# Optimization experiments

Hardware: AMD Instinct MI355X
Metric: run time of the kernel (lower is better)

Reference implementation:

```python
import jax, jax.numpy as jnp
import numpy as np

NP, NC, F, H = 50000, 10000, 128, 256
E_ANNO, E_LINK, E_PPI, NPAIR = 250000, 100000, 500000, 4096


def _sage(x_src, x_dst, src, dst, Wl, b, Wr):
    # PyG SAGEConv(aggr='mean'): lin_l(mean of gathered neighbor feats) + lin_r(x_dst)
    n_dst = x_dst.shape[0]
    agg = jax.ops.segment_sum(x_src[src], dst, num_segments=n_dst)
    cnt = jax.ops.segment_sum(jnp.ones((src.shape[0], 1), x_src.dtype), dst, num_segments=n_dst)
    mean = agg / jnp.maximum(cnt, 1.0)  # isolated dst nodes get 0
    return mean @ Wl.T + b + x_dst @ Wr.T


def setup_inputs():
    key = jax.random.key(0)
    ks = iter(jax.random.split(key, 64))
    s = 0.05
    inp = {}
    inp['x_protein'] = jax.random.normal(next(ks), (NP, F), jnp.float32)
    inp['x_class'] = jax.random.normal(next(ks), (NC, F), jnp.float32)
    for layer, din, dout in [('a', F, H), ('b', H, F)]:
        for rel in ['annop', 'annon', 'link', 'ppi']:
            inp[f'{layer}_{rel}_Wl'] = jax.random.normal(next(ks), (dout, din), jnp.float32) * s
            inp[f'{layer}_{rel}_b'] = jax.random.normal(next(ks), (dout,), jnp.float32) * s
            inp[f'{layer}_{rel}_Wr'] = jax.random.normal(next(ks), (dout, din), jnp.float32) * s
    inp['lin_W'] = jax.random.normal(next(ks), (1, 2 * F), jnp.float32) * s
    inp['lin_b'] = jnp.zeros((1,), jnp.float32)
    inp['annop_src'] = jax.random.randint(next(ks), (E_ANNO,), 0, NP)
    inp['annop_dst'] = jax.random.randint(next(ks), (E_ANNO,), 0, NC)
    inp['annon_src'] = jax.random.randint(next(ks), (E_ANNO,), 0, NP)
    inp['annon_dst'] = jax.random.randint(next(ks), (E_ANNO,), 0, NC)
    inp['link_src'] = jax.random.randint(next(ks), (E_LINK,), 0, NC)
    inp['link_dst'] = jax.random.randint(next(ks), (E_LINK,), 0, NC)
    inp['ppi_src'] = jax.random.randint(next(ks), (E_PPI,), 0, NP)
    inp['ppi_dst'] = jax.random.randint(next(ks), (E_PPI,), 0, NP)
    inp['mask'] = jax.random.randint(next(ks), (NPAIR, 2), 0, NP)
    return inp


def reference(x_protein, x_class,
              a_annop_Wl, a_annop_b, a_annop_Wr,
              a_annon_Wl, a_annon_b, a_annon_Wr,
              a_link_Wl, a_link_b, a_link_Wr,
              a_ppi_Wl, a_ppi_b, a_ppi_Wr,
              b_annop_Wl, b_annop_b, b_annop_Wr,
              b_annon_Wl, b_annon_b, b_annon_Wr,
              b_link_Wl, b_link_b, b_link_Wr,
              b_ppi_Wl, b_ppi_b, b_ppi_Wr,
              lin_W, lin_b,
              annop_src, annop_dst, annon_src, annon_dst,
              link_src, link_dst, ppi_src, ppi_dst, mask):
    # Layer 1 (HeteroConv aggregates per dst node type with sum)
    hc = (_sage(x_protein, x_class, annop_src, annop_dst, a_annop_Wl, a_annop_b, a_annop_Wr)
          + _sage(x_protein, x_class, annon_src, annon_dst, a_annon_Wl, a_annon_b, a_annon_Wr)
          + _sage(x_class, x_class, link_src, link_dst, a_link_Wl, a_link_b, a_link_Wr))
    hp = _sage(x_protein, x_protein, ppi_src, ppi_dst, a_ppi_Wl, a_ppi_b, a_ppi_Wr)
    hc = jax.nn.relu(hc)
    hp = jax.nn.relu(hp)
    # Layer 2
    hp2 = _sage(hp, hp, ppi_src, ppi_dst, b_ppi_Wl, b_ppi_b, b_ppi_Wr)
    # (class outputs of layer 2 are computed in the original but unused for the head)
    hc2 = (_sage(hp, hc, annop_src, annop_dst, b_annop_Wl, b_annop_b, b_annop_Wr)
           + _sage(hp, hc, annon_src, annon_dst, b_annon_Wl, b_annon_b, b_annon_Wr)
           + _sage(hc, hc, link_src, link_dst, b_link_Wl, b_link_b, b_link_Wr))
    del hc2
    # Pair readout: mask.T -> rows of protein indices; original detaches p1, p2
    p1 = jax.lax.stop_gradient(hp2[mask[:, 0]])
    p2 = jax.lax.stop_gradient(hp2[mask[:, 1]])
    h = jnp.concatenate((p1, p2), axis=1)  # [NPAIR, 2F]
    return jax.nn.sigmoid(h @ lin_W.T + lin_b)
```

## Files before the change

kernel.cpp:

```cpp
#include <hip/hip_runtime.h>
#include <math.h>

#define NPROT 50000
#define NPROT_PAD 50048
#define EPPI 500000
#define NPAIR 4096

typedef __attribute__((ext_vector_type(8))) __bf16 bf16x8;
typedef __attribute__((ext_vector_type(4))) __bf16 bf16x4;
typedef __attribute__((ext_vector_type(4))) float floatx4;

__global__ void k_prep(const float* __restrict__ x,
                       const float* __restrict__ Wl, const float* __restrict__ Wr,
                       const float* __restrict__ linW, const float* __restrict__ linb,
                       const float* __restrict__ bWl, const float* __restrict__ bWr,
                       const float* __restrict__ bb,
                       __bf16* __restrict__ Xb, __bf16* __restrict__ Bw,
                       float* __restrict__ P, float* __restrict__ biasC,
                       int* __restrict__ head) {
    int b = blockIdx.x, t = threadIdx.x;
    if (b < 6250) {
        int i = b * 256 + t;
        int row = i >> 5, k4 = (i & 31) << 2;
        float4 v = *(const float4*)(x + (size_t)row * 128 + k4);
        bf16x4 o; o[0] = (__bf16)v.x; o[1] = (__bf16)v.y; o[2] = (__bf16)v.z; o[3] = (__bf16)v.w;
        *(bf16x4*)(Xb + (size_t)row * 128 + k4) = o;
    } else if (b < 6506) {
        int idx = (b - 6250) * 256 + t;
        int h = idx >> 8, k = idx & 255;
        float v = (k < 128) ? Wl[h * 128 + k] : Wr[h * 128 + (k - 128)];
        Bw[idx] = (__bf16)v;
    } else if (b == 6506) {
        int h = t;
        float v1 = 0, v2 = 0, u1 = 0, u2 = 0;
        for (int f = 0; f < 128; f++) {
            float w1 = linW[f], w2 = linW[128 + f];
            float wl = bWl[f * 256 + h], wr = bWr[f * 256 + h];
            v1 += w1 * wl; v2 += w2 * wl; u1 += w1 * wr; u2 += w2 * wr;
        }
        P[h * 4 + 0] = v1; P[h * 4 + 1] = v2; P[h * 4 + 2] = u1; P[h * 4 + 3] = u2;
        if (h == 0) {
            float c = linb[0];
            for (int f = 0; f < 128; f++) c += (linW[f] + linW[128 + f]) * bb[f];
            *biasC = c;
        }
    } else {
        int i = (b - 6507) * 256 + t;
        if (i < NPROT) head[i] = -1;
    }
}

__global__ void k_link(const int* __restrict__ src, const int* __restrict__ dst,
                       int* __restrict__ head, int2* __restrict__ elist) {
    int e = blockIdx.x * 256 + threadIdx.x;
    if (e < EPPI) {
        int d = dst[e];
        int prev = atomicExch(&head[d], e);
        elist[e] = make_int2(src[e], prev);
    }
}

__global__ void k_agg(const __bf16* __restrict__ Xb, const int* __restrict__ head,
                      const int2* __restrict__ elist, float* __restrict__ inv,
                      __bf16* __restrict__ Am) {
    int wave = threadIdx.x >> 6, lane = threadIdx.x & 63;
    int q = lane >> 4, sl = lane & 15;
    int node = blockIdx.x * 16 + wave * 4 + q;
    if (node >= NPROT) return;
    float a[8];
#pragma unroll
    for (int e8 = 0; e8 < 8; e8++) a[e8] = 0.f;
    const __bf16* base = Xb + (size_t)sl * 8;
    int e = head[node];
    int c = 0;
    while (e >= 0) {
        int2 el = elist[e];
        bf16x8 v = *(const bf16x8*)(base + (size_t)el.x * 128);
#pragma unroll
        for (int e8 = 0; e8 < 8; e8++) a[e8] += (float)v[e8];
        c++;
        e = el.y;
    }
    float iv = 1.0f / (float)(c > 1 ? c : 1);
    if (sl == 0 && q == 0) {  }
    if (sl == 0) inv[node] = iv;
    bf16x8 o;
#pragma unroll
    for (int e8 = 0; e8 < 8; e8++) o[e8] = (__bf16)(a[e8] * iv);
    *(bf16x8*)(Am + (size_t)node * 128 + sl * 8) = o;
}

__global__ __launch_bounds__(256) void k_gemm(const __bf16* __restrict__ Am,
                                              const __bf16* __restrict__ Xb,
                                              const __bf16* __restrict__ Bw,
                                              const float* __restrict__ ab,
                                              const float* __restrict__ P,
                                              float* __restrict__ y) {
    __shared__ __bf16 Bs[2048 * 8];
    int tid = threadIdx.x;
    int wave = tid >> 6, lane = tid & 63;
    int r = lane & 15, quad = lane >> 4;
    int row0 = blockIdx.x * 128 + wave * 32;

    bf16x8 afrag[2][8];
#pragma unroll
    for (int g = 0; g < 2; g++) {
        const __bf16* mp = Am + (size_t)(row0 + g * 16 + r) * 128 + quad * 8;
        const __bf16* op = Xb + (size_t)(row0 + g * 16 + r) * 128 + quad * 8;
#pragma unroll
        for (int kk = 0; kk < 4; kk++) {
            afrag[g][kk]     = *(const bf16x8*)(mp + kk * 32);
            afrag[g][4 + kk] = *(const bf16x8*)(op + kk * 32);
        }
    }

    float part[2][4][4] = {{{0.f}}};

    for (int chunk = 0; chunk < 4; chunk++) {
        if (chunk) __syncthreads();
#pragma unroll
        for (int jj = 0; jj < 8; jj++) {
            int g = jj * 256 + tid;
            int gr = g & 15, gq = (g >> 4) & 3;
            int gkk = (g >> 6) & 7;
            int gt = g >> 9;
            const __bf16* src = Bw + (size_t)(chunk * 64 + gt * 16 + gr) * 256 + gkk * 32 + gq * 8;
            *(bf16x8*)(Bs + (size_t)g * 8) = *(const bf16x8*)src;
        }
        __syncthreads();

        floatx4 acc[2][4];
#pragma unroll
        for (int g = 0; g < 2; g++)
#pragma unroll
            for (int t = 0; t < 4; t++) acc[g][t] = (floatx4){0.f, 0.f, 0.f, 0.f};
#pragma unroll
        for (int kk = 0; kk < 8; kk++) {
#pragma unroll
            for (int t = 0; t < 4; t++) {
                bf16x8 bf = *(const bf16x8*)(Bs + (size_t)((t * 8 + kk) * 64 + lane) * 8);
                acc[0][t] = __builtin_amdgcn_mfma_f32_16x16x32_bf16(afrag[0][kk], bf, acc[0][t], 0, 0, 0);
                acc[1][t] = __builtin_amdgcn_mfma_f32_16x16x32_bf16(afrag[1][kk], bf, acc[1][t], 0, 0, 0);
            }
        }

#pragma unroll
        for (int t = 0; t < 4; t++) {
            int col = chunk * 64 + t * 16 + r;
            float bias = ab[col];
            float4 pv = *(const float4*)(P + col * 4);
#pragma unroll
            for (int g = 0; g < 2; g++)
#pragma unroll
                for (int rr = 0; rr < 4; rr++) {
                    float h = acc[g][t][rr] + bias;
                    h = h > 0.f ? h : 0.f;
                    part[g][rr][0] += h * pv.x; part[g][rr][1] += h * pv.y;
                    part[g][rr][2] += h * pv.z; part[g][rr][3] += h * pv.w;
                }
        }
    }

#pragma unroll
    for (int m = 1; m < 16; m <<= 1)
#pragma unroll
        for (int g = 0; g < 2; g++)
#pragma unroll
            for (int rr = 0; rr < 4; rr++)
#pragma unroll
                for (int j = 0; j < 4; j++)
                    part[g][rr][j] += __shfl_xor(part[g][rr][j], m, 64);
    if (r == 0) {
#pragma unroll
        for (int g = 0; g < 2; g++)
#pragma unroll
            for (int rr = 0; rr < 4; rr++) {
                int row = row0 + g * 16 + quad * 4 + rr;
                float4 o;
                o.x = part[g][rr][0]; o.y = part[g][rr][1];
                o.z = part[g][rr][2]; o.w = part[g][rr][3];
                *(float4*)(y + (size_t)row * 4) = o;
            }
    }
}

__global__ void k_head(const int* __restrict__ mask, const int* __restrict__ head,
                       const int2* __restrict__ elist, const float* __restrict__ y,
                       const float* __restrict__ biasC, float* __restrict__ out) {
    int tid = blockIdx.x * 256 + threadIdx.x;
    int p = tid >> 1, side = tid & 1;
    float res = 0.f;
    if (p < NPAIR) {
        int node = mask[p * 2 + side];
        int e = head[node];
        float s = 0.f;
        int c = 0;
        while (e >= 0) {
            int2 el = elist[e];
            s += y[(size_t)el.x * 4 + side];
            c++;
            e = el.y;
        }
        float iv = 1.0f / (float)(c > 1 ? c : 1);
        res = s * iv + y[(size_t)node * 4 + 2 + side];
    }
    float other = __shfl_xor(res, 1, 64);
    if (p < NPAIR && side == 0) {
        float z = res + other + *biasC;
        out[p] = 1.f / (1.f + expf(-z));
    }
}

extern "C" void kernel_launch(void* const* d_in, const int* in_sizes, int n_in,
                              void* d_out, int out_size, void* d_ws, size_t ws_size,
                              hipStream_t stream) {
    const float* x_protein = (const float*)d_in[0];
    const float* a_ppi_Wl  = (const float*)d_in[11];
    const float* a_ppi_b   = (const float*)d_in[12];
    const float* a_ppi_Wr  = (const float*)d_in[13];
    const float* b_ppi_Wl  = (const float*)d_in[23];
    const float* b_ppi_b   = (const float*)d_in[24];
    const float* b_ppi_Wr  = (const float*)d_in[25];
    const float* lin_W     = (const float*)d_in[26];
    const float* lin_b     = (const float*)d_in[27];
    const int* ppi_src     = (const int*)d_in[34];
    const int* ppi_dst     = (const int*)d_in[35];
    const int* mask        = (const int*)d_in[36];
    float* out = (float*)d_out;

    char* ws = (char*)d_ws;
    size_t o = 0;
    auto alloc = [&](size_t n) -> char* {
        char* r = ws + o;
        o = (o + n + 511) & ~(size_t)511;
        return r;
    };
    int*    head   = (int*)alloc((size_t)NPROT * 4);
    int2*   elist  = (int2*)alloc((size_t)EPPI * 8);
    float*  inv    = (float*)alloc((size_t)NPROT * 4);
    __bf16* Xb     = (__bf16*)alloc((size_t)NPROT_PAD * 128 * 2);
    __bf16* Am     = (__bf16*)alloc((size_t)NPROT_PAD * 128 * 2);
    __bf16* Bw     = (__bf16*)alloc(256 * 256 * 2);
    float*  P      = (float*)alloc(256 * 4 * 4);
    float*  biasC  = (float*)alloc(4);
    float*  y      = (float*)alloc((size_t)NPROT_PAD * 4 * 4);
    (void)ws_size;

    k_prep<<<6703, 256, 0, stream>>>(x_protein, a_ppi_Wl, a_ppi_Wr, lin_W, lin_b,
                                     b_ppi_Wl, b_ppi_Wr, b_ppi_b,
                                     Xb, Bw, P, biasC, head);
    k_link<<<(EPPI + 255) / 256, 256, 0, stream>>>(ppi_src, ppi_dst, head, elist);
    k_agg<<<(NPROT + 15) / 16, 256, 0, stream>>>(Xb, head, elist, inv, Am);
    k_gemm<<<(NPROT_PAD + 127) / 128, 256, 0, stream>>>(Am, Xb, Bw, a_ppi_b, P, y);
    k_head<<<(2 * NPAIR + 255) / 256, 256, 0, stream>>>(mask, head, elist, y, biasC, out);
}
```

Measured before the change: 242.6 us.

## Parallelize head-weight projection, drop unused inv buffer, load GEMM weights direct to LDS

The single-block serial loop computing the folded layer-2/readout projection P and biasC is spread across 256 blocks, one per hidden unit, using wave shuffles and a shared-memory reduction. This removes a long serial tail block from the prep kernel. The unused per-node inverse-count store in the aggregation kernel is also removed. The GEMM's weight staging now uses global_load_lds to copy straight into LDS without passing through registers, though that path depends on the LDS destination layout matching what the builtin writes per lane.

```diff
diff --git a/kernel.cpp b/kernel.cpp
--- a/kernel.cpp
+++ b/kernel.cpp
@@ -18,6 +18,7 @@
                        __bf16* __restrict__ Xb, __bf16* __restrict__ Bw,
                        float* __restrict__ P, float* __restrict__ biasC,
                        int* __restrict__ head) {
+    __shared__ float sP[10];
     int b = blockIdx.x, t = threadIdx.x;
     if (b < 6250) {
         int i = b * 256 + t;
@@ -30,22 +31,35 @@
         int h = idx >> 8, k = idx & 255;
         float v = (k < 128) ? Wl[h * 128 + k] : Wr[h * 128 + (k - 128)];
         Bw[idx] = (__bf16)v;
-    } else if (b == 6506) {
-        int h = t;
-        float v1 = 0, v2 = 0, u1 = 0, u2 = 0;
-        for (int f = 0; f < 128; f++) {
-            float w1 = linW[f], w2 = linW[128 + f];
-            float wl = bWl[f * 256 + h], wr = bWr[f * 256 + h];
-            v1 += w1 * wl; v2 += w2 * wl; u1 += w1 * wr; u2 += w2 * wr;
-        }
-        P[h * 4 + 0] = v1; P[h * 4 + 1] = v2; P[h * 4 + 2] = u1; P[h * 4 + 3] = u2;
-        if (h == 0) {
-            float c = linb[0];
-            for (int f = 0; f < 128; f++) c += (linW[f] + linW[128 + f]) * bb[f];
-            *biasC = c;
+    } else if (b < 6762) {
+        int h = b - 6506;
+        int lane = t & 63, wave = t >> 6;
+        float v1 = 0, v2 = 0, u1 = 0, u2 = 0, c = 0;
+        if (t < 128) {
+            float w1 = linW[t], w2 = linW[128 + t];
+            float wl = bWl[t * 256 + h], wr = bWr[t * 256 + h];
+            v1 = w1 * wl; v2 = w2 * wl; u1 = w1 * wr; u2 = w2 * wr;
+            if (h == 0) c = (w1 + w2) * bb[t];
+        }
+#pragma unroll
+        for (int m = 1; m < 64; m <<= 1) {
+            v1 += __shfl_xor(v1, m, 64); v2 += __shfl_xor(v2, m, 64);
+            u1 += __shfl_xor(u1, m, 64); u2 += __shfl_xor(u2, m, 64);
+            c  += __shfl_xor(c, m, 64);
+        }
+        if (lane == 0 && wave < 2) {
+            sP[wave * 5 + 0] = v1; sP[wave * 5 + 1] = v2;
+            sP[wave * 5 + 2] = u1; sP[wave * 5 + 3] = u2;
+            sP[wave * 5 + 4] = c;
+        }
+        __syncthreads();
+        if (t == 0) {
+            P[h * 4 + 0] = sP[0] + sP[5]; P[h * 4 + 1] = sP[1] + sP[6];
+            P[h * 4 + 2] = sP[2] + sP[7]; P[h * 4 + 3] = sP[3] + sP[8];
+            if (h == 0) *biasC = linb[0] + sP[4] + sP[9];
         }
     } else {
-        int i = (b - 6507) * 256 + t;
+        int i = (b - 6762) * 256 + t;
         if (i < NPROT) head[i] = -1;
     }
 }
@@ -61,8 +75,7 @@
 }
 
 __global__ void k_agg(const __bf16* __restrict__ Xb, const int* __restrict__ head,
-                      const int2* __restrict__ elist, float* __restrict__ inv,
-                      __bf16* __restrict__ Am) {
+                      const int2* __restrict__ elist, __bf16* __restrict__ Am) {
     int wave = threadIdx.x >> 6, lane = threadIdx.x & 63;
     int q = lane >> 4, sl = lane & 15;
     int node = blockIdx.x * 16 + wave * 4 + q;
@@ -82,8 +95,6 @@
         e = el.y;
     }
     float iv = 1.0f / (float)(c > 1 ? c : 1);
-    if (sl == 0 && q == 0) {  }
-    if (sl == 0) inv[node] = iv;
     bf16x8 o;
 #pragma unroll
     for (int e8 = 0; e8 < 8; e8++) o[e8] = (__bf16)(a[e8] * iv);
@@ -125,7 +136,10 @@
             int gkk = (g >> 6) & 7;
             int gt = g >> 9;
             const __bf16* src = Bw + (size_t)(chunk * 64 + gt * 16 + gr) * 256 + gkk * 32 + gq * 8;
-            *(bf16x8*)(Bs + (size_t)g * 8) = *(const bf16x8*)src;
+            __builtin_amdgcn_global_load_lds(
+                (const __attribute__((address_space(1))) void*)src,
+                (__attribute__((address_space(3))) void*)(Bs + (size_t)g * 8),
+                16, 0, 0);
         }
         __syncthreads();
 
@@ -237,7 +251,6 @@
     };
     int*    head   = (int*)alloc((size_t)NPROT * 4);
     int2*   elist  = (int2*)alloc((size_t)EPPI * 8);
-    float*  inv    = (float*)alloc((size_t)NPROT * 4);
     __bf16* Xb     = (__bf16*)alloc((size_t)NPROT_PAD * 128 * 2);
     __bf16* Am     = (__bf16*)alloc((size_t)NPROT_PAD * 128 * 2);
     __bf16* Bw     = (__bf16*)alloc(256 * 256 * 2);
@@ -246,11 +259,11 @@
     float*  y      = (float*)alloc((size_t)NPROT_PAD * 4 * 4);
     (void)ws_size;
 
-    k_prep<<<6703, 256, 0, stream>>>(x_protein, a_ppi_Wl, a_ppi_Wr, lin_W, lin_b,
+    k_prep<<<6958, 256, 0, stream>>>(x_protein, a_ppi_Wl, a_ppi_Wr, lin_W, lin_b,
                                      b_ppi_Wl, b_ppi_Wr, b_ppi_b,
                                      Xb, Bw, P, biasC, head);
     k_link<<<(EPPI + 255) / 256, 256, 0, stream>>>(ppi_src, ppi_dst, head, elist);
-    k_agg<<<(NPROT + 15) / 16, 256, 0, stream>>>(Xb, head, elist, inv, Am);
+    k_agg<<<(NPROT + 15) / 16, 256, 0, stream>>>(Xb, head, elist, Am);
     k_gemm<<<(NPROT_PAD + 127) / 128, 256, 0, stream>>>(Am, Xb, Bw, a_ppi_b, P, y);
     k_head<<<(2 * NPAIR + 255) / 256, 256, 0, stream>>>(mask, head, elist, y, biasC, out);
 }
```

After: 241.5 us. No clear change (-0.4%).
